# Kernel optimization log

Measured on AMD Instinct MI355X. Metric: run time of the kernel, lower is better.

The kernel has to match this reference:

```python
import jax, jax.numpy as jnp
import numpy as np

VOCAB, EMBED, HIDDEN, OUT = 32000, 300, 512, 7


def setup_inputs() -> dict:
    key = jax.random.key(0)
    ks = jax.random.split(key, 8)
    tokens = jax.random.randint(ks[0], (256, 512), 0, VOCAB, dtype=jnp.int32)
    # embedding table (padding_idx=0 row zeroed inside reference)
    emb = jax.random.normal(ks[1], (VOCAB, EMBED), dtype=jnp.float32)
    # xavier-uniform-like init for recurrent weights
    lim_ih = float(np.sqrt(6.0 / (EMBED + 4 * HIDDEN)))
    lim_hh = float(np.sqrt(6.0 / (HIDDEN + 4 * HIDDEN)))
    W_ih = jax.random.uniform(ks[2], (4 * HIDDEN, EMBED), jnp.float32, -lim_ih, lim_ih)
    W_hh = jax.random.uniform(ks[3], (4 * HIDDEN, HIDDEN), jnp.float32, -lim_hh, lim_hh)
    b_ih = jax.random.uniform(ks[4], (4 * HIDDEN,), jnp.float32, -0.05, 0.05)
    b_hh = jax.random.uniform(ks[5], (4 * HIDDEN,), jnp.float32, -0.05, 0.05)
    lim_fc = float(np.sqrt(1.0 / HIDDEN))
    W_fc = jax.random.uniform(ks[6], (OUT, HIDDEN), jnp.float32, -lim_fc, lim_fc)
    b_fc = jax.random.uniform(ks[7], (OUT,), jnp.float32, -lim_fc, lim_fc)
    return {"tokens": tokens, "emb": emb, "W_ih": W_ih, "b_ih": b_ih,
            "W_hh": W_hh, "b_hh": b_hh, "W_fc": W_fc, "b_fc": b_fc}


def reference(tokens, emb, W_ih, b_ih, W_hh, b_hh, W_fc, b_fc):
    B, S = tokens.shape
    H = W_hh.shape[1]
    # padding_idx=0: row 0 of the embedding table is zero
    emb = emb.at[0].set(0.0)
    x_emb = emb[tokens]  # [B, S, E]
    # precompute input projections for all timesteps in one GEMM
    gx = jnp.einsum('bse,ge->bsg', x_emb, W_ih) + b_ih  # [B, S, 4H]
    gx_t = jnp.moveaxis(gx, 1, 0)  # [S, B, 4H]

    def step(carry, g_x):
        h, c = carry
        gates = g_x + h @ W_hh.T + b_hh  # [B, 4H]
        i_g, f_g, g_g, o_g = jnp.split(gates, 4, axis=1)
        i = jax.nn.sigmoid(i_g)
        f = jax.nn.sigmoid(f_g)
        g = jnp.tanh(g_g)
        o = jax.nn.sigmoid(o_g)
        c_next = f * c + i * g
        h_next = o * jnp.tanh(c_next)
        return (h_next, c_next), None

    h0 = jnp.zeros((B, H), dtype=x_emb.dtype)
    c0 = jnp.zeros((B, H), dtype=x_emb.dtype)
    (h_T, _), _ = jax.lax.scan(step, (h0, c0), gx_t)
    # dropout is identity in eval mode
    logits = h_T @ W_fc.T + b_fc  # [B, OUT]
    return logits
```

## Files before the change

kernel.cpp:

```cpp
#include <hip/hip_runtime.h>
#include <hip/hip_bf16.h>


typedef unsigned short ushort_t;
typedef unsigned long long u64_t;
typedef __bf16 bf16x8 __attribute__((ext_vector_type(8)));
typedef unsigned short u16x8v __attribute__((ext_vector_type(8)));
typedef float f32x4 __attribute__((ext_vector_type(4)));

#define U_STRIDE 840
#define HOFF 320
#define SCR_S 36

__device__ __forceinline__ float sigmoidf_(float x) { return 1.0f / (1.0f + __expf(-x)); }
__device__ __forceinline__ float tanhf_(float x)    { return 1.0f - 2.0f / (__expf(2.0f * x) + 1.0f); }

__device__ __forceinline__ ushort_t f2bf(float f) {
    unsigned u = __builtin_bit_cast(unsigned, f);
    unsigned r = (u + 0x7FFFu + ((u >> 16) & 1u)) >> 16;
    return (ushort_t)r;
}
__device__ __forceinline__ float bf2f(ushort_t u) {
    unsigned v = ((unsigned)u) << 16;
    return __builtin_bit_cast(float, v);
}

__device__ __forceinline__ u64_t g_load64(const u64_t* p) {
    return __hip_atomic_load(p, __ATOMIC_RELAXED, __HIP_MEMORY_SCOPE_AGENT);
}
__device__ __forceinline__ void g_store64(u64_t* p, u64_t v) {
    __hip_atomic_store(p, v, __ATOMIC_RELAXED, __HIP_MEMORY_SCOPE_AGENT);
}
__device__ __forceinline__ int g_load_flag(const int* p) {
    return __hip_atomic_load(p, __ATOMIC_RELAXED, __HIP_MEMORY_SCOPE_AGENT);
}
__device__ __forceinline__ void g_store_flag(int* p, int v) {
    __hip_atomic_store(p, v, __ATOMIC_RELAXED, __HIP_MEMORY_SCOPE_AGENT);
}

__global__ __launch_bounds__(256, 1)
void lstm_fused_kernel(const int* __restrict__ tokens,
                       const float* __restrict__ emb,
                       const float* __restrict__ Wih,
                       const float* __restrict__ bih,
                       const float* __restrict__ Whh,
                       const float* __restrict__ bhh,
                       const float* __restrict__ Wfc,
                       const float* __restrict__ bfc,
                       float* __restrict__ out,
                       int* __restrict__ flags,
                       ushort_t* __restrict__ hbuf)
{
    __shared__ ushort_t u_lds[16 * U_STRIDE];
    __shared__ ushort_t h_scr[16 * SCR_S];

    const int tid = threadIdx.x;
    const int bid = blockIdx.x;
    const int g   = bid & 15;
    const int ib  = bid >> 4;
    const int Bg0 = g * 16;
    const int U0  = ib * 32;
    const int lane = tid & 63;
    const int wv   = tid >> 6;
    const int lm   = lane & 15;
    const int q    = lane >> 4;

    bf16x8 aih[2][10];
    bf16x8 ahh[2][16];
#pragma unroll
    for (int m = 0; m < 2; ++m) {
        const int rp   = 32 * wv + 16 * m + lm;
        const int gi   = rp & 3;
        const int up   = rp >> 2;
        const int grow = gi * 512 + U0 + up;
#pragma unroll
        for (int kc = 0; kc < 10; ++kc) {
            u16x8v tmp;
#pragma unroll
            for (int j = 0; j < 8; ++j) {
                int col = 32 * kc + 8 * q + j;
                tmp[j] = (col < 300) ? f2bf(Wih[grow * 300 + col]) : (ushort_t)0;
            }
            aih[m][kc] = __builtin_bit_cast(bf16x8, tmp);
        }
#pragma unroll
        for (int kc = 0; kc < 16; ++kc) {
            u16x8v tmp;
#pragma unroll
            for (int j = 0; j < 8; ++j) {
                int col = 32 * kc + 8 * q + j;
                tmp[j] = f2bf(Whh[grow * 512 + col]);
            }
            ahh[m][kc] = __builtin_bit_cast(bf16x8, tmp);
        }
    }

    float bias[2][4];
#pragma unroll
    for (int m = 0; m < 2; ++m) {
        const int unit = U0 + 8 * wv + 4 * m + q;
#pragma unroll
        for (int j = 0; j < 4; ++j)
            bias[m][j] = bih[j * 512 + unit] + bhh[j * 512 + unit];
    }

    if (tid < 128) {
        int r = tid >> 3;
        int d = tid & 7;
        g_store64((u64_t*)(hbuf + (size_t)(Bg0 + r) * 512 + U0 + 4 * d), 0ull);
    }
    __syncthreads();
    if (tid == 0) g_store_flag(&flags[g * 16 + ib], 1);

    const int* myflag = &flags[g * 16 + (lane & 15)];
    float c0 = 0.0f, c1 = 0.0f;

    const int xr  = tid >> 4;
    const int xln = tid & 15;
    const int xb  = Bg0 + xr;
    int tok_cur = tokens[xb * 512 + 0];
    int tok_nxt = tokens[xb * 512 + 1];
    float2 xp[10];
    {
        const float2* s2 = (const float2*)(emb + (size_t)tok_cur * 300);
#pragma unroll
        for (int k = 0; k < 10; ++k) {
            int i = xln + 16 * k;
            if (i < 150) xp[k] = s2[i];
        }
    }

    for (int t = 0; t < 512; ++t) {
        {
            unsigned int* dstx = (unsigned int*)(u_lds + xr * U_STRIDE);
            const bool tz = (tok_cur != 0);
#pragma unroll
            for (int k = 0; k < 10; ++k) {
                int i = xln + 16 * k;
                unsigned int v = 0u;
                if (tz && i < 150)
                    v = (unsigned int)f2bf(xp[k].x) | ((unsigned int)f2bf(xp[k].y) << 16);
                dstx[i] = v;
            }
        }
        __syncthreads();

        {
            tok_cur = tok_nxt;
            const float2* s2 = (const float2*)(emb + (size_t)tok_cur * 300);
#pragma unroll
            for (int k = 0; k < 10; ++k) {
                int i = xln + 16 * k;
                if (i < 150) xp[k] = s2[i];
            }
            int t2 = (t + 2 < 512) ? (t + 2) : 511;
            tok_nxt = tokens[xb * 512 + t2];
        }

        f32x4 acc0 = {0.f, 0.f, 0.f, 0.f};
        f32x4 acc1 = {0.f, 0.f, 0.f, 0.f};
        const ushort_t* u0 = u_lds + lm * U_STRIDE + 8 * q;
#pragma unroll
        for (int kc = 0; kc < 10; ++kc) {
            bf16x8 b0 = __builtin_bit_cast(bf16x8, *(const u16x8v*)(u0 + 32 * kc));
            acc0 = __builtin_amdgcn_mfma_f32_16x16x32_bf16(aih[0][kc], b0, acc0, 0, 0, 0);
            acc1 = __builtin_amdgcn_mfma_f32_16x16x32_bf16(aih[1][kc], b0, acc1, 0, 0, 0);
        }

        if (wv == 0) {
            const int target = t + 1;
            while (true) {
                int v = g_load_flag(myflag);
                if (__all(v >= target)) break;
                __builtin_amdgcn_s_sleep(1);
            }
            asm volatile("" ::: "memory");
        }
        __syncthreads();

        {
            const int r  = tid >> 4;
            const int ln = tid & 15;
            const u64_t* hsrc = (const u64_t*)(hbuf + (size_t)(t & 1) * (256 * 512)
                                               + (size_t)(Bg0 + r) * 512);
            u64_t* dsth = (u64_t*)(u_lds + r * U_STRIDE + HOFF);
            u64_t tmp[8];
#pragma unroll
            for (int k = 0; k < 8; ++k) tmp[k] = g_load64(hsrc + ln + 16 * k);
#pragma unroll
            for (int k = 0; k < 8; ++k) dsth[ln + 16 * k] = tmp[k];
        }
        __syncthreads();

#pragma unroll
        for (int kc = 0; kc < 16; ++kc) {
            bf16x8 b0 = __builtin_bit_cast(bf16x8, *(const u16x8v*)(u0 + HOFF + 32 * kc));
            acc0 = __builtin_amdgcn_mfma_f32_16x16x32_bf16(ahh[0][kc], b0, acc0, 0, 0, 0);
            acc1 = __builtin_amdgcn_mfma_f32_16x16x32_bf16(ahh[1][kc], b0, acc1, 0, 0, 0);
        }

        {
            {
                float ig = sigmoidf_(acc0.x + bias[0][0]);
                float fg = sigmoidf_(acc0.y + bias[0][1]);
                float gg = tanhf_(acc0.z + bias[0][2]);
                float og = sigmoidf_(acc0.w + bias[0][3]);
                c0 = fg * c0 + ig * gg;
                h_scr[lm * SCR_S + 8 * wv + q] = f2bf(og * tanhf_(c0));
            }
            {
                float ig = sigmoidf_(acc1.x + bias[1][0]);
                float fg = sigmoidf_(acc1.y + bias[1][1]);
                float gg = tanhf_(acc1.z + bias[1][2]);
                float og = sigmoidf_(acc1.w + bias[1][3]);
                c1 = fg * c1 + ig * gg;
                h_scr[lm * SCR_S + 8 * wv + 4 + q] = f2bf(og * tanhf_(c1));
            }
        }
        __syncthreads();

        if (tid < 128) {
            const int r = tid >> 3;
            const int d = tid & 7;
            u64_t v = *(const u64_t*)((const char*)h_scr + r * (SCR_S * 2) + d * 8);
            ushort_t* hdst = hbuf + (size_t)((t + 1) & 1) * (256 * 512);
            g_store64((u64_t*)(hdst + (size_t)(Bg0 + r) * 512 + U0 + 4 * d), v);
        }
        __syncthreads();
        if (tid == 0) g_store_flag(&flags[g * 16 + ib], t + 2);
    }

    if (wv == 0) {
        while (true) {
            int v = g_load_flag(myflag);
            if (__all(v >= 513)) break;
            __builtin_amdgcn_s_sleep(1);
        }
        asm volatile("" ::: "memory");
    }
    __syncthreads();

    {
        const int bb = Bg0 + ib;
        const ushort_t* hrow = hbuf + (size_t)bb * 512;
        u64_t h0 = g_load64((const u64_t*)(hrow + lane * 8));
        u64_t h1 = g_load64((const u64_t*)(hrow + lane * 8 + 4));
        float hv[8];
#pragma unroll
        for (int j = 0; j < 4; ++j) hv[j]     = bf2f((ushort_t)(h0 >> (16 * j)));
#pragma unroll
        for (int j = 0; j < 4; ++j) hv[4 + j] = bf2f((ushort_t)(h1 >> (16 * j)));
#pragma unroll
        for (int oo = 0; oo < 2; ++oo) {
            int o = wv + 4 * oo;
            if (o < 7) {
                f32x4 w0 = *(const f32x4*)(Wfc + o * 512 + lane * 8);
                f32x4 w1 = *(const f32x4*)(Wfc + o * 512 + lane * 8 + 4);
                float s = hv[0] * w0.x + hv[1] * w0.y + hv[2] * w0.z + hv[3] * w0.w
                        + hv[4] * w1.x + hv[5] * w1.y + hv[6] * w1.z + hv[7] * w1.w;
#pragma unroll
                for (int sh = 32; sh >= 1; sh >>= 1) s += __shfl_down(s, sh);
                if (lane == 0)
                    out[bb * 7 + o] = s + bfc[o];
            }
        }
    }
}

extern "C" void kernel_launch(void* const* d_in, const int* in_sizes, int n_in,
                              void* d_out, int out_size, void* d_ws, size_t ws_size,
                              hipStream_t stream) {
    const int* tokens = (const int*)d_in[0];
    const float* emb  = (const float*)d_in[1];
    const float* Wih  = (const float*)d_in[2];
    const float* bih  = (const float*)d_in[3];
    const float* Whh  = (const float*)d_in[4];
    const float* bhh  = (const float*)d_in[5];
    const float* Wfc  = (const float*)d_in[6];
    const float* bfc  = (const float*)d_in[7];

    int* flags      = (int*)d_ws;
    ushort_t* hbuf  = (ushort_t*)((char*)d_ws + 1024);

    lstm_fused_kernel<<<dim3(256), dim3(256), 0, stream>>>(
        tokens, emb, Wih, bih, Whh, bhh, Wfc, bfc,
        (float*)d_out, flags, hbuf);
}
```

Before: 1.550 ms.

## Use per-wave flags and direct h stores to drop block barriers

```diff
diff --git a/kernel.cpp b/kernel.cpp
--- a/kernel.cpp
+++ b/kernel.cpp
@@ -10,7 +10,6 @@
 
 #define U_STRIDE 840
 #define HOFF 320
-#define SCR_S 36
 
 __device__ __forceinline__ float sigmoidf_(float x) { return 1.0f / (1.0f + __expf(-x)); }
 __device__ __forceinline__ float tanhf_(float x)    { return 1.0f - 2.0f / (__expf(2.0f * x) + 1.0f); }
@@ -29,6 +28,9 @@
     return __hip_atomic_load(p, __ATOMIC_RELAXED, __HIP_MEMORY_SCOPE_AGENT);
 }
 __device__ __forceinline__ void g_store64(u64_t* p, u64_t v) {
+    __hip_atomic_store(p, v, __ATOMIC_RELAXED, __HIP_MEMORY_SCOPE_AGENT);
+}
+__device__ __forceinline__ void g_store32(unsigned int* p, unsigned int v) {
     __hip_atomic_store(p, v, __ATOMIC_RELAXED, __HIP_MEMORY_SCOPE_AGENT);
 }
 __device__ __forceinline__ int g_load_flag(const int* p) {
@@ -52,7 +54,6 @@
                        ushort_t* __restrict__ hbuf)
 {
     __shared__ ushort_t u_lds[16 * U_STRIDE];
-    __shared__ ushort_t h_scr[16 * SCR_S];
 
     const int tid = threadIdx.x;
     const int bid = blockIdx.x;
@@ -69,10 +70,7 @@
     bf16x8 ahh[2][16];
 #pragma unroll
     for (int m = 0; m < 2; ++m) {
-        const int rp   = 32 * wv + 16 * m + lm;
-        const int gi   = rp & 3;
-        const int up   = rp >> 2;
-        const int grow = gi * 512 + U0 + up;
+        const int grow = (lm & 3) * 512 + U0 + 8 * wv + 2 * (lm >> 2) + m;
 #pragma unroll
         for (int kc = 0; kc < 10; ++kc) {
             u16x8v tmp;
@@ -98,7 +96,7 @@
     float bias[2][4];
 #pragma unroll
     for (int m = 0; m < 2; ++m) {
-        const int unit = U0 + 8 * wv + 4 * m + q;
+        const int unit = U0 + 8 * wv + 2 * q + m;
 #pragma unroll
         for (int j = 0; j < 4; ++j)
             bias[m][j] = bih[j * 512 + unit] + bhh[j * 512 + unit];
@@ -110,9 +108,10 @@
         g_store64((u64_t*)(hbuf + (size_t)(Bg0 + r) * 512 + U0 + 4 * d), 0ull);
     }
     __syncthreads();
-    if (tid == 0) g_store_flag(&flags[g * 16 + ib], 1);
-
-    const int* myflag = &flags[g * 16 + (lane & 15)];
+    if (lane == 0) g_store_flag(&flags[g * 64 + ib * 4 + wv], 1);
+
+    const int* myflag = &flags[g * 64 + lane];
+    int* pubflag = &flags[g * 64 + ib * 4 + wv];
     float c0 = 0.0f, c1 = 0.0f;
 
     const int xr  = tid >> 4;
@@ -167,7 +166,7 @@
             acc1 = __builtin_amdgcn_mfma_f32_16x16x32_bf16(aih[1][kc], b0, acc1, 0, 0, 0);
         }
 
-        if (wv == 0) {
+        {
             const int target = t + 1;
             while (true) {
                 int v = g_load_flag(myflag);
@@ -176,7 +175,6 @@
             }
             asm volatile("" ::: "memory");
         }
-        __syncthreads();
 
         {
             const int r  = tid >> 4;
@@ -200,13 +198,14 @@
         }
 
         {
+            float h0v, h1v;
             {
                 float ig = sigmoidf_(acc0.x + bias[0][0]);
                 float fg = sigmoidf_(acc0.y + bias[0][1]);
                 float gg = tanhf_(acc0.z + bias[0][2]);
                 float og = sigmoidf_(acc0.w + bias[0][3]);
                 c0 = fg * c0 + ig * gg;
-                h_scr[lm * SCR_S + 8 * wv + q] = f2bf(og * tanhf_(c0));
+                h0v = og * tanhf_(c0);
             }
             {
                 float ig = sigmoidf_(acc1.x + bias[1][0]);
@@ -214,23 +213,18 @@
                 float gg = tanhf_(acc1.z + bias[1][2]);
                 float og = sigmoidf_(acc1.w + bias[1][3]);
                 c1 = fg * c1 + ig * gg;
-                h_scr[lm * SCR_S + 8 * wv + 4 + q] = f2bf(og * tanhf_(c1));
-            }
-        }
-        __syncthreads();
-
-        if (tid < 128) {
-            const int r = tid >> 3;
-            const int d = tid & 7;
-            u64_t v = *(const u64_t*)((const char*)h_scr + r * (SCR_S * 2) + d * 8);
+                h1v = og * tanhf_(c1);
+            }
+            unsigned int hp = (unsigned int)f2bf(h0v) | ((unsigned int)f2bf(h1v) << 16);
             ushort_t* hdst = hbuf + (size_t)((t + 1) & 1) * (256 * 512);
-            g_store64((u64_t*)(hdst + (size_t)(Bg0 + r) * 512 + U0 + 4 * d), v);
-        }
-        __syncthreads();
-        if (tid == 0) g_store_flag(&flags[g * 16 + ib], t + 2);
-    }
-
-    if (wv == 0) {
+            g_store32((unsigned int*)(hdst + (size_t)(Bg0 + lm) * 512 + U0 + 8 * wv + 2 * q),
+                      hp);
+        }
+        asm volatile("s_waitcnt vmcnt(0)" ::: "memory");
+        if (lane == 0) g_store_flag(pubflag, t + 2);
+    }
+
+    {
         while (true) {
             int v = g_load_flag(myflag);
             if (__all(v >= 513)) break;
@@ -238,7 +232,6 @@
         }
         asm volatile("" ::: "memory");
     }
-    __syncthreads();
 
     {
         const int bb = Bg0 + ib;
@@ -280,7 +273,7 @@
     const float* bfc  = (const float*)d_in[7];
 
     int* flags      = (int*)d_ws;
-    ushort_t* hbuf  = (ushort_t*)((char*)d_ws + 1024);
+    ushort_t* hbuf  = (ushort_t*)((char*)d_ws + 4096);
 
     lstm_fused_kernel<<<dim3(256), dim3(256), 0, stream>>>(
         tokens, emb, Wih, bih, Whh, bhh, Wfc, bfc,
```

Result: slower. 1.682 ms (+8.5%).
